# Kernel tuning notes

Hardware: AMD Instinct MI355X
Metric: run time of the kernel (lower is better)

## Reference

```python
import jax, jax.numpy as jnp
import numpy as np

G, KP, EPS = 4, 9, 1e-5  # deformable groups, 3x3 kernel points, BN eps


def setup_inputs() -> dict:
    key = jax.random.key(0)
    ks = jax.random.split(key, 16)
    N, C1, C2, H, W = 8, 256, 256, 64, 64
    c = int(C1 * 1.0) // 16 * 16  # 256 internal width
    OM = int(np.ceil(G * KP * 3 / 8) * 8)  # 112 padded offset/mask dim (108 used)
    sd = 0.02
    return {
        "x": jax.random.normal(ks[0], (N, C1, H, W), jnp.float32),
        "cv1_w": jax.random.normal(ks[1], (c, C1), jnp.float32) * sd,
        "cv1_b": jax.random.normal(ks[2], (c,), jnp.float32) * sd,
        "value_w": jax.random.normal(ks[3], (c, c), jnp.float32) * sd,
        "value_b": jax.random.normal(ks[4], (c,), jnp.float32) * sd,
        "dw_w": jax.random.normal(ks[5], (c,), jnp.float32) * sd + 1.0,
        "dw_b": jax.random.normal(ks[6], (c,), jnp.float32) * sd,
        "om_w": jax.random.normal(ks[7], (OM, c), jnp.float32) * sd,
        "om_b": jax.random.normal(ks[8], (OM,), jnp.float32) * sd,
        "out_w": jax.random.normal(ks[9], (c, c), jnp.float32) * sd,
        "cv2_w": jax.random.normal(ks[10], (C2, c), jnp.float32) * sd,
        "bn_gamma": jnp.ones((C2,), jnp.float32),
        "bn_beta": jnp.zeros((C2,), jnp.float32),
        "bn_mean": jax.random.normal(ks[11], (C2,), jnp.float32) * 0.1,
        "bn_var": jax.random.uniform(ks[12], (C2,), jnp.float32, minval=0.5, maxval=1.5),
    }


def _dcnv4(value, offset_mask, H, W):
    """DCNv4 core: offset-based bilinear sampling + unnormalized-mask aggregation.
    value: (N,H,W,c) NHWC features; offset_mask: (N,H,W,OM), per group layout
    [2*KP offsets (dx,dy pairs), KP masks]; no softmax on masks (DCNv4)."""
    N, c = value.shape[0], value.shape[-1]
    GC = c // G
    om = offset_mask[..., : G * KP * 3].reshape(N, H, W, G, 3 * KP)
    offs = om[..., : 2 * KP].reshape(N, H, W, G, KP, 2)  # (dx, dy), x = width axis
    mask = om[..., 2 * KP:]                               # (N,H,W,G,KP)
    ky, kx = jnp.meshgrid(jnp.arange(-1, 2, dtype=jnp.float32),
                          jnp.arange(-1, 2, dtype=jnp.float32), indexing="ij")
    kx, ky = kx.reshape(KP), ky.reshape(KP)               # 3x3 dilation-1 grid
    base_x = jnp.arange(W, dtype=jnp.float32)[None, None, :, None, None]
    base_y = jnp.arange(H, dtype=jnp.float32)[None, :, None, None, None]
    px = base_x + kx + offs[..., 0]                       # (N,H,W,G,KP) abs pixel x
    py = base_y + ky + offs[..., 1]
    x0, y0 = jnp.floor(px), jnp.floor(py)
    fx, fy = px - x0, py - y0
    x0i, y0i = x0.astype(jnp.int32), y0.astype(jnp.int32)
    vflat = value.reshape(N, H * W, G, GC).transpose(0, 2, 1, 3)  # (N,G,L,GC)
    acc = jnp.zeros((N, G, H, W, KP, GC), value.dtype)
    for dy, dx, wgt in ((0, 0, (1 - fy) * (1 - fx)), (0, 1, (1 - fy) * fx),
                        (1, 0, fy * (1 - fx)), (1, 1, fy * fx)):
        yy, xx = y0i + dy, x0i + dx
        valid = (yy >= 0) & (yy < H) & (xx >= 0) & (xx < W)   # zero padding
        idx = jnp.clip(yy, 0, H - 1) * W + jnp.clip(xx, 0, W - 1)
        idx_g = idx.transpose(0, 3, 1, 2, 4).reshape(N, G, H * W * KP)
        smp = jnp.take_along_axis(vflat, idx_g[..., None], axis=2)
        smp = smp.reshape(N, G, H, W, KP, GC)
        acc = acc + smp * (wgt * valid).transpose(0, 3, 1, 2, 4)[..., None]
    out = (acc * mask.transpose(0, 3, 1, 2, 4)[..., None]).sum(axis=4)  # (N,G,H,W,GC)
    return out.transpose(0, 2, 3, 1, 4).reshape(N, H, W, c)


def reference(x, cv1_w, cv1_b, value_w, value_b, dw_w, dw_b, om_w, om_b,
              out_w, cv2_w, bn_gamma, bn_beta, bn_mean, bn_var):
    N, C1, H, W = x.shape
    t = jnp.einsum("nchw,dc->nhwd", x, cv1_w) + cv1_b       # cv1 1x1 conv -> NHWC
    value = t @ value_w.T + value_b                          # DCNv4 value_proj
    om = (t * dw_w + dw_b) @ om_w.T + om_b                   # depthwise 1x1 + linear
    y = _dcnv4(value, om, H, W)
    y = y @ out_w.T                                          # output_proj (no bias)
    y = jnp.einsum("nhwc,dc->nhwd", y, cv2_w)                # cv2 1x1 (no bias)
    y = (y - bn_mean) * bn_gamma * jax.lax.rsqrt(bn_var + EPS) + bn_beta  # BN (eval)
    y = y * jax.nn.sigmoid(y)                                # SiLU
    return y.transpose(0, 3, 1, 2)                           # back to NCHW
```

## Files before the change

### kernel.cpp

```cpp
#include <hip/hip_runtime.h>
#include <hip/hip_bf16.h>
#include <math.h>

#define NN    8
#define HH    64
#define WW    64
#define HW    4096
#define NHW   32768
#define EPSBN 1e-5f

#define PCELLS   4624
#define PELEMS   295936
#define ROWS68   4352

typedef __attribute__((ext_vector_type(8))) short short8v;
typedef __attribute__((ext_vector_type(4))) float f32x4;
typedef __attribute__((ext_vector_type(2))) float f32x2;

__device__ __forceinline__ float b2f(unsigned short u) {
    union { unsigned int i; float f; } v; v.i = ((unsigned int)u) << 16; return v.f;
}
__device__ __forceinline__ unsigned short f2b(float f) {
    __hip_bfloat16 h = __float2bfloat16(f);
    return *reinterpret_cast<const unsigned short*>(&h);
}
__device__ __forceinline__ f32x2 bf2x(int u) {
    union { int i; float f; } a, b;
    a.i = u << 16;
    b.i = u & 0xffff0000;
    f32x2 r; r[0] = a.f; r[1] = b.f; return r;
}


__global__ __launch_bounds__(256)
void prep_all_kernel(const float* __restrict__ cv1_w, const float* __restrict__ cv1_b,
                     const float* __restrict__ value_w, const float* __restrict__ value_b,
                     const float* __restrict__ dw_w, const float* __restrict__ dw_b,
                     const float* __restrict__ om_w, const float* __restrict__ om_b,
                     const float* __restrict__ out_w, const float* __restrict__ cv2_w,
                     const float* __restrict__ bn_g, const float* __restrict__ bn_b,
                     const float* __restrict__ bn_m, const float* __restrict__ bn_v,
                     unsigned short* __restrict__ Wallbf, float* __restrict__ ball,
                     unsigned short* __restrict__ Woutbf, float* __restrict__ bout,
                     unsigned short* __restrict__ V2)
{
    int bid = blockIdx.x;
    int t = threadIdx.x;

    if (bid < 40) {
        __shared__ float As[16][64];
        __shared__ float Bs[16][64];
        int kind, m0, n0;
        if (bid < 16)      { kind = 0; m0 = (bid >> 2) * 64;        n0 = (bid & 3) * 64; }
        else if (bid < 24) { kind = 1; m0 = ((bid - 16) >> 2) * 64; n0 = ((bid - 16) & 3) * 64; }
        else               { kind = 2; m0 = ((bid - 24) >> 2) * 64; n0 = ((bid - 24) & 3) * 64; }

        const float* A = (kind == 0) ? value_w : (kind == 1) ? om_w : cv2_w;
        const float* B = (kind == 2) ? out_w : cv1_w;

        int am = t >> 2, ak4 = (t & 3) * 4;
        int bk = t >> 4, bn4 = (t & 15) * 4;

        float acc[4][4] = {};
        int px = (t & 15) << 2;
        int dx = (t >> 4) << 2;

        for (int c0 = 0; c0 < 256; c0 += 16) {
            float4 av;
            if (kind == 1 && (m0 + am) >= 112) {
                av = float4{0.f, 0.f, 0.f, 0.f};
            } else {
                av = *reinterpret_cast<const float4*>(&A[(size_t)(m0 + am) * 256 + c0 + ak4]);
                if (kind == 1) {
                    float4 dv = *reinterpret_cast<const float4*>(&dw_w[c0 + ak4]);
                    av.x *= dv.x; av.y *= dv.y; av.z *= dv.z; av.w *= dv.w;
                }
            }
            As[ak4 + 0][am] = av.x;
            As[ak4 + 1][am] = av.y;
            As[ak4 + 2][am] = av.z;
            As[ak4 + 3][am] = av.w;
            *reinterpret_cast<float4*>(&Bs[bk][bn4]) =
                *reinterpret_cast<const float4*>(&B[(size_t)(c0 + bk) * 256 + n0 + bn4]);
            __syncthreads();
            #pragma unroll
            for (int k = 0; k < 16; ++k) {
                float4 a = *reinterpret_cast<const float4*>(&As[k][px]);
                float4 b = *reinterpret_cast<const float4*>(&Bs[k][dx]);
                float avv[4] = {a.x, a.y, a.z, a.w};
                float bvv[4] = {b.x, b.y, b.z, b.w};
                #pragma unroll
                for (int i = 0; i < 4; ++i)
                    #pragma unroll
                    for (int j = 0; j < 4; ++j)
                        acc[i][j] = fmaf(avv[i], bvv[j], acc[i][j]);
            }
            __syncthreads();
        }

        #pragma unroll
        for (int i = 0; i < 4; ++i) {
            int m = m0 + px + i;
            if (kind == 1 && m >= 112) continue;
            float sc = 1.f;
            if (kind == 2) sc = bn_g[m] * rsqrtf(bn_v[m] + EPSBN);
            #pragma unroll
            for (int j = 0; j < 4; ++j) {
                float v = acc[i][j] * sc;
                int cc = n0 + dx + j;
                if (kind == 0)      Wallbf[m * 256 + cc] = f2b(v);
                else if (kind == 1) Wallbf[(256 + m) * 256 + cc] = f2b(v);
                else                Woutbf[m * 256 + cc] = f2b(v);
            }
        }
    } else if (bid == 40) {
        int d = t;
        float s = value_b[d];
        for (int e = 0; e < 256; ++e) s = fmaf(value_w[d*256+e], cv1_b[e], s);
        ball[d] = s;
    } else if (bid == 41) {
        if (t < 112) {
            float s = om_b[t];
            for (int e = 0; e < 256; ++e)
                s = fmaf(om_w[t*256+e], fmaf(dw_w[e], cv1_b[e], dw_b[e]), s);
            ball[256 + t] = s;
        } else if (t < 128) {
            ball[256 + t] = 0.f;
        }
        short8v z = {};
        *reinterpret_cast<short8v*>(&Wallbf[368*256 + t*16]) = z;
        *reinterpret_cast<short8v*>(&Wallbf[368*256 + t*16 + 8]) = z;
    } else if (bid == 42) {
        float sc = bn_g[t] * rsqrtf(bn_v[t] + EPSBN);
        bout[t] = fmaf(-bn_m[t], sc, bn_b[t]);
    } else {
        int pb = bid - 43;
        unsigned short* base = V2 + (size_t)(pb >> 3) * PELEMS;
        int off = (pb & 7) * 528;
        for (int ii = t; ii < 528; ii += 256) {
            int idx = off + ii;
            int cellsub = idx >> 3;
            int chunk = idx & 7;
            int cell;
            if (cellsub < 272) {
                int r = cellsub / 68;
                int c = cellsub - r * 68;
                int row = (r < 2) ? r : r + 62;
                cell = row * 68 + c;
            } else {
                int i2 = cellsub - 272;
                int row = 2 + (i2 >> 2);
                int cs = i2 & 3;
                int col = (cs < 2) ? cs : cs + 62;
                cell = row * 68 + col;
            }
            *reinterpret_cast<int4*>(&base[cell * 64 + chunk * 8]) = int4{0,0,0,0};
        }
    }
}

__global__ __launch_bounds__(256)
void gemm_vo_kernel(const float* __restrict__ x, const unsigned short* __restrict__ Wallbf,
                    const float* __restrict__ ball,
                    unsigned short* __restrict__ V2, unsigned short* __restrict__ OM)
{
    __shared__ unsigned short As[8192];
    __shared__ unsigned short Bs[8192];
    int t = threadIdx.x;
    int m0 = blockIdx.y * 128;
    int n0 = blockIdx.x * 128;
    int nimg = m0 >> 12, hw0 = m0 & 4095;
    int lane = t & 63;
    int wv = t >> 6;
    int wr = wv >> 1, wc = wv & 1;
    int r_l = lane & 15, kg_l = lane >> 4;
    int ci = t >> 6;
    int l  = t & 63;

    const float* xbase = x + (size_t)(nimg * 256) * 4096 + hw0;

    f32x4 acc[4][4] = {};

    for (int kt = 0; kt < 4; ++kt) {
        int c0 = kt * 64;
        float2 val[16];
        #pragma unroll
        for (int i = 0; i < 16; ++i)
            val[i] = *reinterpret_cast<const float2*>(
                &xbase[(size_t)(c0 + ci*16 + i) * 4096 + 2*l]);
        __syncthreads();
        #pragma unroll
        for (int rsel = 0; rsel < 2; ++rsel) {
            int row = 2*l + rsel;
            #pragma unroll
            for (int kgi = 0; kgi < 2; ++kgi) {
                int kg = ci*2 + kgi;
                short8v s;
                #pragma unroll
                for (int j = 0; j < 8; ++j)
                    s[j] = (short)f2b(rsel ? val[kgi*8+j].y : val[kgi*8+j].x);
                *reinterpret_cast<short8v*>(&As[row*64 + ((kg ^ (row & 7)) << 3)]) = s;
            }
        }
        #pragma unroll
        for (int i = 0; i < 4; ++i) {
            int idx = t + i*256;
            int row = idx >> 3, kg = idx & 7;
            *reinterpret_cast<short8v*>(&Bs[row*64 + ((kg ^ (row & 7)) << 3)]) =
                *reinterpret_cast<const short8v*>(&Wallbf[(size_t)(n0 + row)*256 + c0 + kg*8]);
        }
        __syncthreads();
        #pragma unroll
        for (int ks = 0; ks < 2; ++ks) {
            short8v af[4], bfr[4];
            #pragma unroll
            for (int m = 0; m < 4; ++m) {
                int row = wr*64 + m*16 + r_l;
                af[m] = *reinterpret_cast<const short8v*>(
                    &As[row*64 + (((ks*4 + kg_l) ^ (row & 7)) << 3)]);
            }
            #pragma unroll
            for (int n = 0; n < 4; ++n) {
                int row = wc*64 + n*16 + r_l;
                bfr[n] = *reinterpret_cast<const short8v*>(
                    &Bs[row*64 + (((ks*4 + kg_l) ^ (row & 7)) << 3)]);
            }
            #pragma unroll
            for (int m = 0; m < 4; ++m)
                #pragma unroll
                for (int n = 0; n < 4; ++n)
                    acc[m][n] = __builtin_amdgcn_mfma_f32_16x16x32_bf16(af[m], bfr[n], acc[m][n], 0, 0, 0);
        }
    }

    #pragma unroll
    for (int n = 0; n < 4; ++n) {
        int d = n0 + wc*64 + n*16 + r_l;
        float bb = ball[d];
        #pragma unroll
        for (int m = 0; m < 4; ++m) {
            int pr = m0 + wr*64 + m*16 + (kg_l << 2);
            #pragma unroll
            for (int r = 0; r < 4; ++r) {
                float res = acc[m][n][r] + bb;
                int p = pr + r;
                if (d < 256) {
                    int g = d >> 6, ch = d & 63;
                    int hw = p & 4095;
                    int yy = hw >> 6, xx = hw & 63;
                    size_t cell = (size_t)((p >> 12)*4 + g) * PCELLS + (yy + 2)*68 + (xx + 2);
                    V2[cell * 64 + ch] = f2b(res);
                } else if (d < 368) {
                    OM[(size_t)p * 112 + (d - 256)] = f2b(res);
                }
            }
        }
    }
}

__device__ __forceinline__
void gemm_mainloop(const unsigned short* __restrict__ A, const unsigned short* __restrict__ B,
                   int m0, int n0, unsigned short* As, unsigned short* Bs,
                   f32x4 (&acc)[4][4], int t)
{
    int lane = t & 63;
    int wv = t >> 6;
    int wr = wv >> 1, wc = wv & 1;
    int r_l = lane & 15;
    int kg_l = lane >> 4;

    for (int kt = 0; kt < 4; ++kt) {
        int c0 = kt * 64;
        #pragma unroll
        for (int i = 0; i < 4; ++i) {
            int idx = t + i * 256;
            int kg = idx & 7, row = idx >> 3;
            int soff = row*64 + ((kg ^ (row & 7)) << 3);
            *reinterpret_cast<short8v*>(&As[soff]) =
                *reinterpret_cast<const short8v*>(&A[(size_t)(m0 + row)*256 + c0 + kg*8]);
            *reinterpret_cast<short8v*>(&Bs[soff]) =
                *reinterpret_cast<const short8v*>(&B[(size_t)(n0 + row)*256 + c0 + kg*8]);
        }
        __syncthreads();
        #pragma unroll
        for (int ks = 0; ks < 2; ++ks) {
            short8v af[4], bfr[4];
            #pragma unroll
            for (int m = 0; m < 4; ++m) {
                int row = wr*64 + m*16 + r_l;
                af[m] = *reinterpret_cast<const short8v*>(
                    &As[row*64 + (((ks*4 + kg_l) ^ (row & 7)) << 3)]);
            }
            #pragma unroll
            for (int n = 0; n < 4; ++n) {
                int row = wc*64 + n*16 + r_l;
                bfr[n] = *reinterpret_cast<const short8v*>(
                    &Bs[row*64 + (((ks*4 + kg_l) ^ (row & 7)) << 3)]);
            }
            #pragma unroll
            for (int m = 0; m < 4; ++m)
                #pragma unroll
                for (int n = 0; n < 4; ++n)
                    acc[m][n] = __builtin_amdgcn_mfma_f32_16x16x32_bf16(af[m], bfr[n], acc[m][n], 0, 0, 0);
        }
        __syncthreads();
    }
}

__global__ __launch_bounds__(256)
void gemm_out_kernel(const unsigned short* __restrict__ Woutbf, const unsigned short* __restrict__ y,
                     const float* __restrict__ bout, float* __restrict__ out)
{
    __shared__ unsigned short lds[2 * 8192];
    int t = threadIdx.x;
    int m0 = blockIdx.x * 128;
    int n0 = blockIdx.y * 128;
    f32x4 acc[4][4] = {};
    gemm_mainloop(Woutbf, y, m0, n0, lds, lds + 8192, acc, t);

    int lane = t & 63;
    int wv = t >> 6, wr = wv >> 1, wc = wv & 1;
    int r_l = lane & 15, kg_l = lane >> 4;
    int nimg = n0 >> 12;
    int hwb = n0 & 4095;
    #pragma unroll
    for (int m = 0; m < 4; ++m) {
        int dbase = m0 + wr*64 + m*16 + (kg_l << 2);
        #pragma unroll
        for (int r = 0; r < 4; ++r) {
            int d = dbase + r;
            float bb = bout[d];
            #pragma unroll
            for (int n = 0; n < 4; ++n) {
                int pcol = wc*64 + n*16 + r_l;
                float z = acc[m][n][r] + bb;
                float sv = z / (1.f + __expf(-z));
                out[((size_t)(nimg*256 + d))*4096 + hwb + pcol] = sv;
            }
        }
    }
}

__global__ __launch_bounds__(256)
void dcn_kernel(const unsigned short* __restrict__ V2, const unsigned short* __restrict__ OM,
                unsigned short* __restrict__ y)
{
    __shared__ float om_s[8][108];
    int t = threadIdx.x;
    int bid = blockIdx.x;
    int logical = ((bid & 7) << 9) + (bid >> 3);
    int p0 = logical * 8;

    for (int i = t; i < 864; i += 256) {
        int pl = i / 108, j = i - pl * 108;
        om_s[pl][j] = b2f(OM[(size_t)(p0 + pl)*112 + j]);
    }
    __syncthreads();

    int g   = t >> 6;
    int pl  = (t >> 3) & 7;
    int ch8 = t & 7;
    int p = p0 + pl;
    int hw = p & 4095;
    int h = hw >> 6, w = hw & 63;
    const unsigned short* plane =
        V2 + (size_t)((p >> 12)*4 + g) * PELEMS + ch8*8;
    const float* o = &om_s[pl][g*27];

    f32x2 acc2[4] = {};
    #pragma unroll
    for (int k = 0; k < 9; ++k) {
        float dxo = o[2*k], dyo = o[2*k+1], m = o[18+k];
        float px = fminf(fmaxf((float)(w + (k % 3) - 1) + dxo, -1.f), 64.f);
        float py = fminf(fmaxf((float)(h + (k / 3) - 1) + dyo, -1.f), 64.f);
        float x0f = floorf(px), y0f = floorf(py);
        float fx = px - x0f, fy = py - y0f;
        float gx = 1.f - fx, gy = 1.f - fy;
        int cell = ((int)y0f + 2) * 68 + ((int)x0f + 2);
        const unsigned short* cp0 = plane + cell * 64;
        const unsigned short* cp1 = cp0 + ROWS68;
        int4 v00 = *reinterpret_cast<const int4*>(cp0);
        int4 v01 = *reinterpret_cast<const int4*>(cp0 + 64);
        int4 v10 = *reinterpret_cast<const int4*>(cp1);
        int4 v11 = *reinterpret_cast<const int4*>(cp1 + 64);
        float gym = gy * m, fym = fy * m;
        float w00 = gym*gx, w01 = gym*fx, w10 = fym*gx, w11 = fym*fx;
        {
            f32x2 W; W[0] = w00; W[1] = w00;
            int a[4] = {v00.x, v00.y, v00.z, v00.w};
            #pragma unroll
            for (int q = 0; q < 4; ++q) acc2[q] += bf2x(a[q]) * W;
        }
        {
            f32x2 W; W[0] = w01; W[1] = w01;
            int a[4] = {v01.x, v01.y, v01.z, v01.w};
            #pragma unroll
            for (int q = 0; q < 4; ++q) acc2[q] += bf2x(a[q]) * W;
        }
        {
            f32x2 W; W[0] = w10; W[1] = w10;
            int a[4] = {v10.x, v10.y, v10.z, v10.w};
            #pragma unroll
            for (int q = 0; q < 4; ++q) acc2[q] += bf2x(a[q]) * W;
        }
        {
            f32x2 W; W[0] = w11; W[1] = w11;
            int a[4] = {v11.x, v11.y, v11.z, v11.w};
            #pragma unroll
            for (int q = 0; q < 4; ++q) acc2[q] += bf2x(a[q]) * W;
        }
    }

    short8v ov;
    #pragma unroll
    for (int q = 0; q < 4; ++q) {
        ov[2*q]   = (short)f2b(acc2[q][0]);
        ov[2*q+1] = (short)f2b(acc2[q][1]);
    }
    *reinterpret_cast<short8v*>(&y[(size_t)p*256 + g*64 + ch8*8]) = ov;
}

extern "C" void kernel_launch(void* const* d_in, const int* in_sizes, int n_in,
                              void* d_out, int out_size, void* d_ws, size_t ws_size,
                              hipStream_t stream) {
    const float* x       = (const float*)d_in[0];
    const float* cv1_w   = (const float*)d_in[1];
    const float* cv1_b   = (const float*)d_in[2];
    const float* value_w = (const float*)d_in[3];
    const float* value_b = (const float*)d_in[4];
    const float* dw_w    = (const float*)d_in[5];
    const float* dw_b    = (const float*)d_in[6];
    const float* om_w    = (const float*)d_in[7];
    const float* om_b    = (const float*)d_in[8];
    const float* out_w   = (const float*)d_in[9];
    const float* cv2_w   = (const float*)d_in[10];
    const float* bn_g    = (const float*)d_in[11];
    const float* bn_b    = (const float*)d_in[12];
    const float* bn_m    = (const float*)d_in[13];
    const float* bn_v    = (const float*)d_in[14];

    char* ws = (char*)d_ws;
    unsigned short* V2     = (unsigned short*)(ws);
    unsigned short* OM     = (unsigned short*)(ws + 18939904);
    unsigned short* y      = (unsigned short*)(ws + 26279936);
    unsigned short* Wallbf = (unsigned short*)(ws + 43057152);
    unsigned short* Woutbf = (unsigned short*)(ws + 43253760);
    float*          ball   = (float*)(ws + 43384832);
    float*          bout   = (float*)(ws + 43386368);
    float* out = (float*)d_out;

    prep_all_kernel<<<299, 256, 0, stream>>>(cv1_w, cv1_b, value_w, value_b, dw_w, dw_b,
                                             om_w, om_b, out_w, cv2_w,
                                             bn_g, bn_b, bn_m, bn_v,
                                             Wallbf, ball, Woutbf, bout, V2);
    gemm_vo_kernel<<<dim3(3, 256), 256, 0, stream>>>(x, Wallbf, ball, V2, OM);
    dcn_kernel<<<4096, 256, 0, stream>>>(V2, OM, y);
    gemm_out_kernel<<<dim3(2, 256), 256, 0, stream>>>(Woutbf, y, bout, out);
}
```

Before: 94.83 us.

## Stage padded value rows in LDS for deformable sampling, with global fallback

The DCN kernel is remapped so each 512-thread block handles one (image, output row, group) triple. It first copies the five padded rows of that group's value plane that sampling can reach into shared memory, using an XOR-swizzled layout to avoid bank conflicts. Bilinear taps whose rows land in the staged window are read from LDS, and only taps outside it fall back to global loads. This replaces repeated per-tap global/L2 gathers with one coalesced tile load per block, at the cost of about 43 KB of LDS per block (lower occupancy) and a divergent branch per tap.

```diff
diff --git a/kernel.cpp b/kernel.cpp
--- a/kernel.cpp
+++ b/kernel.cpp
@@ -341,31 +341,40 @@
     }
 }
 
-__global__ __launch_bounds__(256)
+__global__ __launch_bounds__(512)
 void dcn_kernel(const unsigned short* __restrict__ V2, const unsigned short* __restrict__ OM,
                 unsigned short* __restrict__ y)
 {
-    __shared__ float om_s[8][108];
+    __shared__ unsigned short vs[5 * 68 * 64];
+    __shared__ float om_s[64][27];
     int t = threadIdx.x;
     int bid = blockIdx.x;
-    int logical = ((bid & 7) << 9) + (bid >> 3);
-    int p0 = logical * 8;
-
-    for (int i = t; i < 864; i += 256) {
-        int pl = i / 108, j = i - pl * 108;
-        om_s[pl][j] = b2f(OM[(size_t)(p0 + pl)*112 + j]);
+    int logical = ((bid & 7) << 8) + (bid >> 3);
+    int n = logical >> 8;
+    int rowg = logical & 255;
+    int h = rowg >> 2, g = rowg & 3;
+    int p0 = n * 4096 + h * 64;
+
+    const unsigned short* plane = V2 + (size_t)(n*4 + g) * PELEMS;
+
+    {
+        const int4* src = reinterpret_cast<const int4*>(plane + (size_t)h * ROWS68);
+        for (int i = t; i < 2720; i += 512) {
+            int cell = i >> 3, c8 = i & 7;
+            *reinterpret_cast<int4*>(&vs[cell*64 + ((c8 ^ (cell & 7)) << 3)]) = src[i];
+        }
+    }
+    for (int i = t; i < 1728; i += 512) {
+        int pl = i / 27, j = i - pl * 27;
+        om_s[pl][j] = b2f(OM[(size_t)(p0 + pl)*112 + g*27 + j]);
     }
     __syncthreads();
 
-    int g   = t >> 6;
-    int pl  = (t >> 3) & 7;
-    int ch8 = t & 7;
+    int pl = t >> 3, ch8 = t & 7;
     int p = p0 + pl;
-    int hw = p & 4095;
-    int h = hw >> 6, w = hw & 63;
-    const unsigned short* plane =
-        V2 + (size_t)((p >> 12)*4 + g) * PELEMS + ch8*8;
-    const float* o = &om_s[pl][g*27];
+    int w = pl;
+    const float* o = om_s[pl];
+    const unsigned short* gbase = plane + ch8*8;
 
     f32x2 acc2[4] = {};
     #pragma unroll
@@ -376,13 +385,25 @@
         float x0f = floorf(px), y0f = floorf(py);
         float fx = px - x0f, fy = py - y0f;
         float gx = 1.f - fx, gy = 1.f - fy;
-        int cell = ((int)y0f + 2) * 68 + ((int)x0f + 2);
-        const unsigned short* cp0 = plane + cell * 64;
-        const unsigned short* cp1 = cp0 + ROWS68;
-        int4 v00 = *reinterpret_cast<const int4*>(cp0);
-        int4 v01 = *reinterpret_cast<const int4*>(cp0 + 64);
-        int4 v10 = *reinterpret_cast<const int4*>(cp1);
-        int4 v11 = *reinterpret_cast<const int4*>(cp1 + 64);
+        int x0 = (int)x0f, y0 = (int)y0f;
+        int lr = y0 + 2 - h;
+        int4 v00, v01, v10, v11;
+        if ((unsigned)lr < 4u) {
+            int cA = lr*68 + x0 + 2;
+            int cB = cA + 1, cC = cA + 68, cD = cA + 69;
+            v00 = *reinterpret_cast<const int4*>(&vs[cA*64 + ((ch8 ^ (cA & 7)) << 3)]);
+            v01 = *reinterpret_cast<const int4*>(&vs[cB*64 + ((ch8 ^ (cB & 7)) << 3)]);
+            v10 = *reinterpret_cast<const int4*>(&vs[cC*64 + ((ch8 ^ (cC & 7)) << 3)]);
+            v11 = *reinterpret_cast<const int4*>(&vs[cD*64 + ((ch8 ^ (cD & 7)) << 3)]);
+        } else {
+            int gc = (y0 + 2)*68 + x0 + 2;
+            const unsigned short* cp0 = gbase + gc * 64;
+            const unsigned short* cp1 = cp0 + ROWS68;
+            v00 = *reinterpret_cast<const int4*>(cp0);
+            v01 = *reinterpret_cast<const int4*>(cp0 + 64);
+            v10 = *reinterpret_cast<const int4*>(cp1);
+            v11 = *reinterpret_cast<const int4*>(cp1 + 64);
+        }
         float gym = gy * m, fym = fy * m;
         float w00 = gym*gx, w01 = gym*fx, w10 = fym*gx, w11 = fym*fx;
         {
@@ -454,6 +475,6 @@
                                              bn_g, bn_b, bn_m, bn_v,
                                              Wallbf, ball, Woutbf, bout, V2);
     gemm_vo_kernel<<<dim3(3, 256), 256, 0, stream>>>(x, Wallbf, ball, V2, OM);
-    dcn_kernel<<<4096, 256, 0, stream>>>(V2, OM, y);
+    dcn_kernel<<<2048, 512, 0, stream>>>(V2, OM, y);
     gemm_out_kernel<<<dim3(2, 256), 256, 0, stream>>>(Woutbf, y, bout, out);
 }
```

Result: slower. 131.6 us (+38.8%).
